# Kernel tuning notes

Measured on AMD Instinct MI355X. Metric: run time of the kernel, lower is better.

## Reference

```python
import jax, jax.numpy as jnp
import numpy as np

D_MODEL = 1024
N_HEADS = 16
D_K = D_MODEL // N_HEADS


def setup_inputs() -> dict:
    key = jax.random.key(0)
    ks = jax.random.split(key, 5)
    B, T = 4, 2048
    scale = 1.0 / np.sqrt(D_MODEL)
    return {
        "x": jax.random.normal(ks[0], (B, T, D_MODEL), dtype=jnp.float32),
        "W_q": jax.random.normal(ks[1], (D_MODEL, D_MODEL), dtype=jnp.float32) * scale,
        "W_k": jax.random.normal(ks[2], (D_MODEL, D_MODEL), dtype=jnp.float32) * scale,
        "W_v": jax.random.normal(ks[3], (D_MODEL, D_MODEL), dtype=jnp.float32) * scale,
        "W_o": jax.random.normal(ks[4], (D_MODEL, D_MODEL), dtype=jnp.float32) * scale,
    }


def reference(x, W_q, W_k, W_v, W_o):
    B, T, C = x.shape
    # torch nn.Linear(bias=False): y = x @ W.T
    def proj(W):
        y = jnp.einsum('btc,dc->btd', x, W)
        # (B, T, H, Dk) -> (B, H, T, Dk)
        return y.reshape(B, T, N_HEADS, D_K).transpose(0, 2, 1, 3)

    Q, K, V = proj(W_q), proj(W_k), proj(W_v)
    scores = jnp.einsum('bhqd,bhkd->bhqk', Q, K) / jnp.sqrt(jnp.float32(D_K))
    # causal mask: disallow k > q
    causal = jnp.triu(jnp.ones((T, T), dtype=bool), k=1)
    scores = jnp.where(causal, -jnp.inf, scores)
    attn = jax.nn.softmax(scores, axis=-1)
    out = jnp.einsum('bhqk,bhkd->bhqd', attn, V)  # (B, H, T, Dk)
    out = out.transpose(0, 2, 1, 3).reshape(B, T, C)
    return jnp.einsum('btc,dc->btd', out, W_o)
```

## Files before the change

kernel.cpp:

```cpp
#include <hip/hip_runtime.h>

typedef unsigned short u16;
typedef __attribute__((ext_vector_type(8))) short short8;
typedef __attribute__((ext_vector_type(4))) float f32x4;
typedef __attribute__((ext_vector_type(16))) float f32x16;

__device__ __forceinline__ u16 f2bf(float f) {
    union { float f; unsigned u; } v; v.f = f;
    unsigned r = v.u + 0x7fff + ((v.u >> 16) & 1);
    return (u16)(r >> 16);
}

__device__ __forceinline__ unsigned cvtpk(float lo, float hi) {
    unsigned r;
    asm("v_cvt_pk_bf16_f32 %0, %1, %2" : "=v"(r) : "v"(lo), "v"(hi));
    return r;
}

__device__ __forceinline__ void plswap(unsigned& a, unsigned& b) {
    auto r = __builtin_amdgcn_permlane32_swap((int)a, (int)b, false, false);
    a = (unsigned)r[0]; b = (unsigned)r[1];
}

__device__ __forceinline__ void gload_lds16(const void* g, void* l) {
    __builtin_amdgcn_global_load_lds(
        (const __attribute__((address_space(1))) void*)g,
        (__attribute__((address_space(3))) void*)l, 16, 0, 0);
}

__global__ __launch_bounds__(256) void cvt_all(
    const float* __restrict__ x, const float* __restrict__ wq, const float* __restrict__ wk,
    const float* __restrict__ wv, const float* __restrict__ wo,
    u16* __restrict__ xb, u16* __restrict__ wqb, u16* __restrict__ wkb,
    u16* __restrict__ wvb, u16* __restrict__ wob)
{
    const int b = blockIdx.x;
    const float* src; u16* dst; int base;
    if (b < 8192)       { src = x;  dst = xb;  base = b; }
    else if (b < 9216)  { src = wq; dst = wqb; base = b - 8192; }
    else if (b < 10240) { src = wk; dst = wkb; base = b - 9216; }
    else if (b < 11264) { src = wv; dst = wvb; base = b - 10240; }
    else                { src = wo; dst = wob; base = b - 11264; }
    const int i = base * 256 + threadIdx.x;
    float4 v = ((const float4*)src)[i];
    ushort4 o;
    o.x = f2bf(v.x); o.y = f2bf(v.y); o.z = f2bf(v.z); o.w = f2bf(v.w);
    ((ushort4*)dst)[i] = o;
}

__global__ __launch_bounds__(256, 2) void gemm_qkv(
    const u16* __restrict__ Agl, const u16* __restrict__ Wq, const u16* __restrict__ Wk,
    const u16* __restrict__ Wv, u16* __restrict__ Qo, u16* __restrict__ Ko, u16* __restrict__ Vo)
{
    __shared__ alignas(16) u16 As[2][128 * 64];
    __shared__ alignas(16) u16 Bs[2][128 * 64];
    const int tid = threadIdx.x;
    const int lane = tid & 63;
    const int w = tid >> 6;
    const int wr = w >> 1, wc = w & 1;
    const int bid = blockIdx.x;
    const int xcd = bid & 7;
    const int j   = bid >> 3;
    const int nb  = j & 7;
    const int rem = j >> 3;
    const int z   = rem >> 3;
    const int yb  = (xcd << 3) | (rem & 7);
    const int m0 = yb * 128;
    const int n0 = nb * 128;
    const u16* Bgl = (z == 0) ? Wq : (z == 1) ? Wk : Wv;

    f32x4 acc[4][4] = {};

    auto stage = [&](int buf, int kb) {
#pragma unroll
        for (int p = 0; p < 4; ++p) {
            const int row = p * 32 + (tid >> 3);
            const int ke = kb + (((tid & 7) * 8) ^ ((row & 7) * 8));
            gload_lds16(Agl + (size_t)(m0 + row) * 1024 + ke, (char*)As[buf] + p * 4096 + w * 1024);
            gload_lds16(Bgl + (size_t)(n0 + row) * 1024 + ke, (char*)Bs[buf] + p * 4096 + w * 1024);
        }
    };

    stage(0, 0);
    for (int kt = 0; kt < 16; ++kt) {
        const int cur = kt & 1;
        if (kt < 15) {
            stage(cur ^ 1, (kt + 1) * 64);
            asm volatile("s_waitcnt vmcnt(8)" ::: "memory");
        } else {
            asm volatile("s_waitcnt vmcnt(0)" ::: "memory");
        }
        __builtin_amdgcn_s_barrier();
        asm volatile("" ::: "memory");
#pragma unroll
        for (int ks = 0; ks < 2; ++ks) {
            short8 a[4], b[4];
#pragma unroll
            for (int m = 0; m < 4; ++m) {
                const int row = wr * 64 + m * 16 + (lane & 15);
                const int ke = (ks * 32 + (lane >> 4) * 8) ^ ((row & 7) * 8);
                a[m] = *(const short8*)(&As[cur][row * 64 + ke]);
            }
#pragma unroll
            for (int n = 0; n < 4; ++n) {
                const int row = wc * 64 + n * 16 + (lane & 15);
                const int ke = (ks * 32 + (lane >> 4) * 8) ^ ((row & 7) * 8);
                b[n] = *(const short8*)(&Bs[cur][row * 64 + ke]);
            }
#pragma unroll
            for (int m = 0; m < 4; ++m)
#pragma unroll
                for (int n = 0; n < 4; ++n)
                    acc[m][n] = __builtin_amdgcn_mfma_f32_16x16x32_bf16(a[m], b[n], acc[m][n], 0, 0, 0);
        }
        asm volatile("" ::: "memory");
        __builtin_amdgcn_s_barrier();
        asm volatile("" ::: "memory");
    }
    const float qs = (z == 0) ? 0.18033688011112043f : 1.0f;
#pragma unroll
    for (int m = 0; m < 4; ++m)
#pragma unroll
        for (int n = 0; n < 4; ++n)
#pragma unroll
            for (int r = 0; r < 4; ++r) {
                const int row = m0 + wr * 64 + m * 16 + ((lane >> 4) << 2) + r;
                const int col = n0 + wc * 64 + n * 16 + (lane & 15);
                const u16 bv = f2bf(acc[m][n][r] * qs);
                const int bb = row >> 11, t = row & 2047, h = col >> 6, dk = col & 63;
                if (z == 2) {
                    Vo[((size_t)(bb * 16 + h) * 64 + dk) * 2048 + t] = bv;
                } else {
                    u16* dst = (z == 0) ? Qo : Ko;
                    dst[(((size_t)(bb * 16 + h) * 2048 + t) << 6) + dk] = bv;
                }
            }
}

__global__ __launch_bounds__(256, 2) void gemm_out(
    const u16* __restrict__ Agl, const u16* __restrict__ Bgl, float* __restrict__ Co)
{
    __shared__ alignas(16) u16 As[2][128 * 64];
    __shared__ alignas(16) u16 Bs[2][128 * 64];
    const int tid = threadIdx.x;
    const int lane = tid & 63;
    const int w = tid >> 6;
    const int wr = w >> 1, wc = w & 1;
    const int bid = blockIdx.x;
    const int xcd = bid & 7;
    const int j   = bid >> 3;
    const int nb  = j & 7;
    const int yb  = (xcd << 3) | (j >> 3);
    const int m0 = yb * 128;
    const int n0 = nb * 128;

    f32x4 acc[4][4] = {};

    auto stage = [&](int buf, int kb) {
#pragma unroll
        for (int p = 0; p < 4; ++p) {
            const int row = p * 32 + (tid >> 3);
            const int ke = kb + (((tid & 7) * 8) ^ ((row & 7) * 8));
            gload_lds16(Agl + (size_t)(m0 + row) * 1024 + ke, (char*)As[buf] + p * 4096 + w * 1024);
            gload_lds16(Bgl + (size_t)(n0 + row) * 1024 + ke, (char*)Bs[buf] + p * 4096 + w * 1024);
        }
    };

    stage(0, 0);
    for (int kt = 0; kt < 16; ++kt) {
        const int cur = kt & 1;
        if (kt < 15) {
            stage(cur ^ 1, (kt + 1) * 64);
            asm volatile("s_waitcnt vmcnt(8)" ::: "memory");
        } else {
            asm volatile("s_waitcnt vmcnt(0)" ::: "memory");
        }
        __builtin_amdgcn_s_barrier();
        asm volatile("" ::: "memory");
#pragma unroll
        for (int ks = 0; ks < 2; ++ks) {
            short8 a[4], b[4];
#pragma unroll
            for (int m = 0; m < 4; ++m) {
                const int row = wr * 64 + m * 16 + (lane & 15);
                const int ke = (ks * 32 + (lane >> 4) * 8) ^ ((row & 7) * 8);
                a[m] = *(const short8*)(&As[cur][row * 64 + ke]);
            }
#pragma unroll
            for (int n = 0; n < 4; ++n) {
                const int row = wc * 64 + n * 16 + (lane & 15);
                const int ke = (ks * 32 + (lane >> 4) * 8) ^ ((row & 7) * 8);
                b[n] = *(const short8*)(&Bs[cur][row * 64 + ke]);
            }
#pragma unroll
            for (int m = 0; m < 4; ++m)
#pragma unroll
                for (int n = 0; n < 4; ++n)
                    acc[m][n] = __builtin_amdgcn_mfma_f32_16x16x32_bf16(a[m], b[n], acc[m][n], 0, 0, 0);
        }
        asm volatile("" ::: "memory");
        __builtin_amdgcn_s_barrier();
        asm volatile("" ::: "memory");
    }
#pragma unroll
    for (int m = 0; m < 4; ++m)
#pragma unroll
        for (int n = 0; n < 4; ++n)
#pragma unroll
            for (int r = 0; r < 4; ++r) {
                const int row = m0 + wr * 64 + m * 16 + ((lane >> 4) << 2) + r;
                const int col = n0 + wc * 64 + n * 16 + (lane & 15);
                Co[(size_t)row * 1024 + col] = acc[m][n][r];
            }
}

__global__ __launch_bounds__(256, 4) void attn_fwd2(
    const u16* __restrict__ Q, const u16* __restrict__ Kg,
    const u16* __restrict__ Vt, u16* __restrict__ O)
{
    __shared__ alignas(16) u16 Ks[2][64 * 64];
    __shared__ alignas(16) u16 Vs[2][64 * 64];
    __shared__ alignas(16) float abuf[4][32];

    const int tid = threadIdx.x;
    const int lane = tid & 63;
    const int w = tid >> 6;
    const int l31 = lane & 31;
    const int hi = lane >> 5;
    const int bid = blockIdx.x;
    const int s  = bid >> 8;
    const int g  = bid & 255;
    const int u  = g >> 3;
    const int bh = ((u & 7) << 3) | (g & 7);
    const int jj = u >> 3;
    const int p  = ((s >> 1) << 2) | jj;
    const int qc = (s & 1) ? p : (15 - p);
    const size_t hb = (size_t)bh << 17;
    const int bb = bh >> 4, h = bh & 15;

    const int q0 = qc * 128;
    const int wq0 = q0 + w * 32;
    const int ntiles = qc * 2 + 2;
    const int qrow = wq0 + l31;

    short8 qf[4];
#pragma unroll
    for (int ks = 0; ks < 4; ++ks)
        qf[ks] = *(const short8*)(&Q[hb + ((size_t)qrow << 6) + ks * 16 + hi * 8]);

    f32x16 o0 = {}, o1 = {};
    float lsum = 0.f;

#pragma unroll
    for (int pp = 0; pp < 2; ++pp) {
        const int c = pp * 256 + tid;
        const int row = c >> 3;
        const int ke = ((c & 7) * 8) ^ ((row & 7) * 8);
        gload_lds16(&Kg[hb + ((size_t)row << 6) + ke], (char*)Ks[0] + pp * 4096 + w * 1024);
        gload_lds16(&Vt[hb + ((size_t)row << 11) + ke], (char*)Vs[0] + pp * 4096 + w * 1024);
    }
    __syncthreads();

    for (int t = 0; t < ntiles; ++t) {
        const int cur = t & 1;
        if (t + 1 < ntiles) {
            const int t0n = (t + 1) * 64;
#pragma unroll
            for (int pp = 0; pp < 2; ++pp) {
                const int c = pp * 256 + tid;
                const int row = c >> 3;
                const int ke = ((c & 7) * 8) ^ ((row & 7) * 8);
                gload_lds16(&Kg[hb + ((size_t)(t0n + row) << 6) + ke], (char*)Ks[cur ^ 1] + pp * 4096 + w * 1024);
                gload_lds16(&Vt[hb + ((size_t)row << 11) + t0n + ke], (char*)Vs[cur ^ 1] + pp * 4096 + w * 1024);
            }
        }
        const int t0 = t * 64;
        if (t0 <= wq0 + 31) {
            const u16* ks_ = Ks[cur];
            const u16* vs_ = Vs[cur];
            const bool full1 = (t0 + 32 <= wq0 + 31);
            f32x16 s0 = {}, s1 = {};
            __builtin_amdgcn_s_setprio(1);
#pragma unroll
            for (int ks = 0; ks < 4; ++ks) {
                const int d0 = ks * 16 + hi * 8;
                const int r0 = l31;
                short8 kf0 = *(const short8*)(&ks_[r0 * 64 + (d0 ^ ((r0 & 7) * 8))]);
                s0 = __builtin_amdgcn_mfma_f32_32x32x16_bf16(kf0, qf[ks], s0, 0, 0, 0);
            }
            if (full1) {
#pragma unroll
                for (int ks = 0; ks < 4; ++ks) {
                    const int d0 = ks * 16 + hi * 8;
                    const int r1 = 32 + l31;
                    short8 kf1 = *(const short8*)(&ks_[r1 * 64 + (d0 ^ ((r1 & 7) * 8))]);
                    s1 = __builtin_amdgcn_mfma_f32_32x32x16_bf16(kf1, qf[ks], s1, 0, 0, 0);
                }
            }
            __builtin_amdgcn_s_setprio(0);
            if (t0 + 63 > wq0) {
#pragma unroll
                for (int r = 0; r < 16; ++r) {
                    const int kva = t0 + (r & 3) + 8 * (r >> 2) + 4 * hi;
                    if (kva > qrow)                s0[r] = -1e30f;
                    if (full1 && kva + 32 > qrow)  s1[r] = -1e30f;
                }
            }
            float rs = 0.f;
            unsigned pwv[16];
            const int nsl = full1 ? 4 : 2;
#pragma unroll
            for (int sl = 0; sl < 4; ++sl) {
                if (sl >= nsl) break;
                float pv[8];
#pragma unroll
                for (int i = 0; i < 8; ++i) {
                    const float sv = (sl < 2) ? s0[(sl & 1) * 8 + i] : s1[(sl & 1) * 8 + i];
                    pv[i] = exp2f(sv);
                    rs += pv[i];
                }
                unsigned w01 = cvtpk(pv[0], pv[1]);
                unsigned w23 = cvtpk(pv[2], pv[3]);
                unsigned w45 = cvtpk(pv[4], pv[5]);
                unsigned w67 = cvtpk(pv[6], pv[7]);
                plswap(w01, w45);
                plswap(w23, w67);
                pwv[sl * 4 + 0] = w01; pwv[sl * 4 + 1] = w23;
                pwv[sl * 4 + 2] = w45; pwv[sl * 4 + 3] = w67;
            }
            rs += __shfl_xor(rs, 32);
            lsum += rs;
            __builtin_amdgcn_s_setprio(1);
#pragma unroll
            for (int sl = 0; sl < 4; ++sl) {
                if (sl >= nsl) break;
                union { unsigned uu4[4]; short8 s8; } uu;
                uu.uu4[0] = pwv[sl * 4 + 0]; uu.uu4[1] = pwv[sl * 4 + 1];
                uu.uu4[2] = pwv[sl * 4 + 2]; uu.uu4[3] = pwv[sl * 4 + 3];
                const int tc = sl * 16 + hi * 8;
                const int r0 = l31, r1 = 32 + l31;
                short8 vf0 = *(const short8*)(&vs_[r0 * 64 + (tc ^ ((r0 & 7) * 8))]);
                short8 vf1 = *(const short8*)(&vs_[r1 * 64 + (tc ^ ((r1 & 7) * 8))]);
                o0 = __builtin_amdgcn_mfma_f32_32x32x16_bf16(uu.s8, vf0, o0, 0, 0, 0);
                o1 = __builtin_amdgcn_mfma_f32_32x32x16_bf16(uu.s8, vf1, o1, 0, 0, 0);
            }
            __builtin_amdgcn_s_setprio(0);
        }
        __syncthreads();
    }
    if (hi == 0) abuf[w][l31] = __builtin_amdgcn_rcpf(lsum);
#pragma unroll
    for (int c = 0; c < 4; ++c) {
        const f32x4 a4 = *(const f32x4*)(&abuf[w][c * 8 + hi * 4]);
#pragma unroll
        for (int e = 0; e < 4; ++e) {
            const int r = c * 4 + e;
            const int qr = wq0 + (r & 3) + 8 * (r >> 2) + 4 * hi;
            const size_t rb = ((size_t)(bb * 2048 + qr) << 10) + h * 64;
            O[rb + l31]      = f2bf(o0[r] * a4[e]);
            O[rb + 32 + l31] = f2bf(o1[r] * a4[e]);
        }
    }
}

extern "C" void kernel_launch(void* const* d_in, const int* in_sizes, int n_in,
                              void* d_out, int out_size, void* d_ws, size_t ws_size,
                              hipStream_t stream) {
    const float* x  = (const float*)d_in[0];
    const float* Wq = (const float*)d_in[1];
    const float* Wk = (const float*)d_in[2];
    const float* Wv = (const float*)d_in[3];
    const float* Wo = (const float*)d_in[4];
    char* ws = (char*)d_ws;
    const size_t MB = 1u << 20;
    u16* xb   = (u16*)(ws);
    u16* Ob   = (u16*)(ws);
    u16* wqb  = (u16*)(ws + 16 * MB);
    u16* wkb  = (u16*)(ws + 18 * MB);
    u16* wvb  = (u16*)(ws + 20 * MB);
    u16* wob  = (u16*)(ws + 22 * MB);
    u16* Qws  = (u16*)(ws + 24 * MB);
    u16* Kws  = (u16*)(ws + 40 * MB);
    u16* Vtws = (u16*)(ws + 56 * MB);

    cvt_all<<<12288, 256, 0, stream>>>(x, Wq, Wk, Wv, Wo, xb, wqb, wkb, wvb, wob);
    gemm_qkv<<<1536, 256, 0, stream>>>(xb, wqb, wkb, wvb, Qws, Kws, Vtws);
    attn_fwd2<<<1024, 256, 0, stream>>>(Qws, Kws, Vtws, Ob);
    gemm_out<<<512, 256, 0, stream>>>(Ob, wob, (float*)d_out);
}
```

Before: 240.3 us.

## Retile QKV GEMM to 256x256 blocks with 512 threads and deeper prefetch

Replaces the 128x128-tile QKV projection kernel with a 256x256-tile version that uses 8 waves per block and 128KB of dynamic LDS. This raises operand reuse per LDS load, cutting global and LDS traffic per FLOP. Global-to-LDS staging now runs two K-steps ahead instead of one, with the refill issued after the post-compute barrier. MFMA bursts are wrapped in s_setprio. The grid shrinks from 1536 to 384 blocks, which risks wave-quantization imbalance across CUs and lowers occupancy, since only one such block fits per CU.

```diff
diff --git a/kernel.cpp b/kernel.cpp
--- a/kernel.cpp
+++ b/kernel.cpp
@@ -48,85 +48,112 @@
     ((ushort4*)dst)[i] = o;
 }
 
-__global__ __launch_bounds__(256, 2) void gemm_qkv(
+__global__ __launch_bounds__(512, 2) void gemm_qkv256(
     const u16* __restrict__ Agl, const u16* __restrict__ Wq, const u16* __restrict__ Wk,
     const u16* __restrict__ Wv, u16* __restrict__ Qo, u16* __restrict__ Ko, u16* __restrict__ Vo)
 {
-    __shared__ alignas(16) u16 As[2][128 * 64];
-    __shared__ alignas(16) u16 Bs[2][128 * 64];
+    extern __shared__ char smem[];
+    char* AsB = smem;
+    char* BsB = smem + 65536;
+
     const int tid = threadIdx.x;
     const int lane = tid & 63;
     const int w = tid >> 6;
-    const int wr = w >> 1, wc = w & 1;
+    const int wr = w >> 2;
+    const int wc = w & 3;
     const int bid = blockIdx.x;
     const int xcd = bid & 7;
     const int j   = bid >> 3;
-    const int nb  = j & 7;
-    const int rem = j >> 3;
-    const int z   = rem >> 3;
-    const int yb  = (xcd << 3) | (rem & 7);
-    const int m0 = yb * 128;
-    const int n0 = nb * 128;
+    const int nb  = j & 3;
+    const int my  = (j >> 2) & 3;
+    const int z   = j >> 4;
+    const int yb  = (xcd << 2) | my;
+    const int m0 = yb * 256;
+    const int n0 = nb * 256;
     const u16* Bgl = (z == 0) ? Wq : (z == 1) ? Wk : Wv;
 
-    f32x4 acc[4][4] = {};
+    f32x4 acc[8][4] = {};
 
     auto stage = [&](int buf, int kb) {
 #pragma unroll
-        for (int p = 0; p < 4; ++p) {
-            const int row = p * 32 + (tid >> 3);
-            const int ke = kb + (((tid & 7) * 8) ^ ((row & 7) * 8));
-            gload_lds16(Agl + (size_t)(m0 + row) * 1024 + ke, (char*)As[buf] + p * 4096 + w * 1024);
-            gload_lds16(Bgl + (size_t)(n0 + row) * 1024 + ke, (char*)Bs[buf] + p * 4096 + w * 1024);
+        for (int g = 0; g < 4; ++g) {
+            const int p = g * 8192 + tid * 16;
+            const int row = p >> 7;
+            const int sg = ((p & 127) >> 4) ^ (row & 7);
+            gload_lds16(Agl + (size_t)(m0 + row) * 1024 + kb + sg * 8, AsB + buf * 32768 + p);
+        }
+#pragma unroll
+        for (int g = 0; g < 4; ++g) {
+            const int p = g * 8192 + tid * 16;
+            const int row = p >> 7;
+            const int sg = ((p & 127) >> 4) ^ (row & 7);
+            gload_lds16(Bgl + (size_t)(n0 + row) * 1024 + kb + sg * 8, BsB + buf * 32768 + p);
         }
     };
 
     stage(0, 0);
+    stage(1, 64);
     for (int kt = 0; kt < 16; ++kt) {
         const int cur = kt & 1;
         if (kt < 15) {
-            stage(cur ^ 1, (kt + 1) * 64);
             asm volatile("s_waitcnt vmcnt(8)" ::: "memory");
         } else {
             asm volatile("s_waitcnt vmcnt(0)" ::: "memory");
         }
         __builtin_amdgcn_s_barrier();
         asm volatile("" ::: "memory");
-#pragma unroll
-        for (int ks = 0; ks < 2; ++ks) {
-            short8 a[4], b[4];
-#pragma unroll
-            for (int m = 0; m < 4; ++m) {
-                const int row = wr * 64 + m * 16 + (lane & 15);
+
+        const u16* Ab = (const u16*)(AsB + cur * 32768);
+        const u16* Bb = (const u16*)(BsB + cur * 32768);
+
+        short8 bfr[4][2];
+#pragma unroll
+        for (int ni = 0; ni < 4; ++ni)
+#pragma unroll
+            for (int ks = 0; ks < 2; ++ks) {
+                const int row = wc * 64 + ni * 16 + (lane & 15);
                 const int ke = (ks * 32 + (lane >> 4) * 8) ^ ((row & 7) * 8);
-                a[m] = *(const short8*)(&As[cur][row * 64 + ke]);
-            }
-#pragma unroll
-            for (int n = 0; n < 4; ++n) {
-                const int row = wc * 64 + n * 16 + (lane & 15);
-                const int ke = (ks * 32 + (lane >> 4) * 8) ^ ((row & 7) * 8);
-                b[n] = *(const short8*)(&Bs[cur][row * 64 + ke]);
-            }
-#pragma unroll
-            for (int m = 0; m < 4; ++m)
-#pragma unroll
-                for (int n = 0; n < 4; ++n)
-                    acc[m][n] = __builtin_amdgcn_mfma_f32_16x16x32_bf16(a[m], b[n], acc[m][n], 0, 0, 0);
-        }
+                bfr[ni][ks] = *(const short8*)(&Bb[row * 64 + ke]);
+            }
+#pragma unroll
+        for (int p = 0; p < 4; ++p) {
+            short8 afr[2][2];
+#pragma unroll
+            for (int mm = 0; mm < 2; ++mm)
+#pragma unroll
+                for (int ks = 0; ks < 2; ++ks) {
+                    const int row = wr * 128 + (p * 2 + mm) * 16 + (lane & 15);
+                    const int ke = (ks * 32 + (lane >> 4) * 8) ^ ((row & 7) * 8);
+                    afr[mm][ks] = *(const short8*)(&Ab[row * 64 + ke]);
+                }
+            __builtin_amdgcn_s_setprio(1);
+#pragma unroll
+            for (int mm = 0; mm < 2; ++mm)
+#pragma unroll
+                for (int ni = 0; ni < 4; ++ni)
+#pragma unroll
+                    for (int ks = 0; ks < 2; ++ks)
+                        acc[p * 2 + mm][ni] = __builtin_amdgcn_mfma_f32_16x16x32_bf16(
+                            afr[mm][ks], bfr[ni][ks], acc[p * 2 + mm][ni], 0, 0, 0);
+            __builtin_amdgcn_s_setprio(0);
+        }
+
         asm volatile("" ::: "memory");
         __builtin_amdgcn_s_barrier();
         asm volatile("" ::: "memory");
+        if (kt + 2 < 16) stage(cur, (kt + 2) * 64);
     }
+
     const float qs = (z == 0) ? 0.18033688011112043f : 1.0f;
 #pragma unroll
-    for (int m = 0; m < 4; ++m)
-#pragma unroll
-        for (int n = 0; n < 4; ++n)
+    for (int mi = 0; mi < 8; ++mi)
+#pragma unroll
+        for (int ni = 0; ni < 4; ++ni)
 #pragma unroll
             for (int r = 0; r < 4; ++r) {
-                const int row = m0 + wr * 64 + m * 16 + ((lane >> 4) << 2) + r;
-                const int col = n0 + wc * 64 + n * 16 + (lane & 15);
-                const u16 bv = f2bf(acc[m][n][r] * qs);
+                const int row = m0 + wr * 128 + mi * 16 + ((lane >> 4) << 2) + r;
+                const int col = n0 + wc * 64 + ni * 16 + (lane & 15);
+                const u16 bv = f2bf(acc[mi][ni][r] * qs);
                 const int bb = row >> 11, t = row & 2047, h = col >> 6, dk = col & 63;
                 if (z == 2) {
                     Vo[((size_t)(bb * 16 + h) * 64 + dk) * 2048 + t] = bv;
@@ -383,8 +410,11 @@
     u16* Kws  = (u16*)(ws + 40 * MB);
     u16* Vtws = (u16*)(ws + 56 * MB);
 
+    hipFuncSetAttribute((const void*)gemm_qkv256,
+                        hipFuncAttributeMaxDynamicSharedMemorySize, 131072);
+
     cvt_all<<<12288, 256, 0, stream>>>(x, Wq, Wk, Wv, Wo, xb, wqb, wkb, wvb, wob);
-    gemm_qkv<<<1536, 256, 0, stream>>>(xb, wqb, wkb, wvb, Qws, Kws, Vtws);
+    gemm_qkv256<<<384, 512, 131072, stream>>>(xb, wqb, wkb, wvb, Qws, Kws, Vtws);
     attn_fwd2<<<1024, 256, 0, stream>>>(Qws, Kws, Vtws, Ob);
     gemm_out<<<512, 256, 0, stream>>>(Ob, wob, (float*)d_out);
 }
```

New measurement: 261.2 us. 1.09x slower.

## Rewrite QKV GEMM with 256x256 tiles, 8 waves and 4-stage LDS pipeline

Applied to the files above, without the earlier changes.

Replaces the 128x128 double-buffered QKV projection GEMM with a 256x256-tile kernel using 512 threads (8 waves), a K-step of 32 and a 4-slot ring buffer in 128KB of dynamic LDS. Global loads for step kt+3 are interleaved between the two MFMA halves of each step, and s_setprio raises priority during MFMA bursts. The aim is more data reuse per tile and better overlap of memory traffic with compute. In exchange it uses large LDS per block with fewer blocks (384), which limits occupancy and may leave CUs underused.

```diff
diff --git a/kernel.cpp b/kernel.cpp
--- a/kernel.cpp
+++ b/kernel.cpp
@@ -48,85 +48,126 @@
     ((ushort4*)dst)[i] = o;
 }
 
-__global__ __launch_bounds__(256, 2) void gemm_qkv(
+__global__ __launch_bounds__(512, 2) void gemm_qkv8p(
     const u16* __restrict__ Agl, const u16* __restrict__ Wq, const u16* __restrict__ Wk,
     const u16* __restrict__ Wv, u16* __restrict__ Qo, u16* __restrict__ Ko, u16* __restrict__ Vo)
 {
-    __shared__ alignas(16) u16 As[2][128 * 64];
-    __shared__ alignas(16) u16 Bs[2][128 * 64];
+    extern __shared__ char smem[];
     const int tid = threadIdx.x;
     const int lane = tid & 63;
     const int w = tid >> 6;
-    const int wr = w >> 1, wc = w & 1;
+    const int wr = w >> 2;
+    const int wc = w & 3;
     const int bid = blockIdx.x;
     const int xcd = bid & 7;
     const int j   = bid >> 3;
-    const int nb  = j & 7;
-    const int rem = j >> 3;
-    const int z   = rem >> 3;
-    const int yb  = (xcd << 3) | (rem & 7);
-    const int m0 = yb * 128;
-    const int n0 = nb * 128;
+    const int my  = j & 3;
+    const int nb  = j >> 2;
+    const int m0  = ((xcd << 2) | my) * 256;
+    const int z   = nb >> 2;
+    const int n0  = (nb & 3) * 256;
     const u16* Bgl = (z == 0) ? Wq : (z == 1) ? Wk : Wv;
 
-    f32x4 acc[4][4] = {};
-
-    auto stage = [&](int buf, int kb) {
-#pragma unroll
-        for (int p = 0; p < 4; ++p) {
-            const int row = p * 32 + (tid >> 3);
-            const int ke = kb + (((tid & 7) * 8) ^ ((row & 7) * 8));
-            gload_lds16(Agl + (size_t)(m0 + row) * 1024 + ke, (char*)As[buf] + p * 4096 + w * 1024);
-            gload_lds16(Bgl + (size_t)(n0 + row) * 1024 + ke, (char*)Bs[buf] + p * 4096 + w * 1024);
+    f32x4 acc[8][4] = {};
+
+    auto stage_kt = [&](int kt, int tensor) {
+        const u16* src = tensor ? Bgl : Agl;
+        const int t0 = tensor ? n0 : m0;
+        char* base = smem + tensor * 65536 + (kt & 3) * 16384;
+#pragma unroll
+        for (int g2 = 0; g2 < 2; ++g2) {
+            const int p = g2 * 8192 + tid * 16;
+            const int rp = p >> 7;
+            const int qs = (p & 127) >> 4;
+            const int lr = qs ^ (rp & 7);
+            const int row = rp * 2 + (lr >> 2);
+            const int ge = (lr & 3) * 8;
+            gload_lds16(src + (size_t)(t0 + row) * 1024 + kt * 32 + ge, base + p);
         }
     };
 
-    stage(0, 0);
-    for (int kt = 0; kt < 16; ++kt) {
-        const int cur = kt & 1;
-        if (kt < 15) {
-            stage(cur ^ 1, (kt + 1) * 64);
-            asm volatile("s_waitcnt vmcnt(8)" ::: "memory");
-        } else {
-            asm volatile("s_waitcnt vmcnt(0)" ::: "memory");
-        }
-        __builtin_amdgcn_s_barrier();
-        asm volatile("" ::: "memory");
-#pragma unroll
-        for (int ks = 0; ks < 2; ++ks) {
-            short8 a[4], b[4];
-#pragma unroll
-            for (int m = 0; m < 4; ++m) {
-                const int row = wr * 64 + m * 16 + (lane & 15);
-                const int ke = (ks * 32 + (lane >> 4) * 8) ^ ((row & 7) * 8);
-                a[m] = *(const short8*)(&As[cur][row * 64 + ke]);
-            }
-#pragma unroll
-            for (int n = 0; n < 4; ++n) {
-                const int row = wc * 64 + n * 16 + (lane & 15);
-                const int ke = (ks * 32 + (lane >> 4) * 8) ^ ((row & 7) * 8);
-                b[n] = *(const short8*)(&Bs[cur][row * 64 + ke]);
-            }
-#pragma unroll
-            for (int m = 0; m < 4; ++m)
-#pragma unroll
-                for (int n = 0; n < 4; ++n)
-                    acc[m][n] = __builtin_amdgcn_mfma_f32_16x16x32_bf16(a[m], b[n], acc[m][n], 0, 0, 0);
-        }
-        asm volatile("" ::: "memory");
-        __builtin_amdgcn_s_barrier();
-        asm volatile("" ::: "memory");
+#define KSTEP(KT, DOSTAGE, VMS)                                                  \
+    {                                                                            \
+        const int slot_ = (KT) & 3;                                              \
+        const u16* Asl = (const u16*)(smem + slot_ * 16384);                     \
+        const u16* Bsl = (const u16*)(smem + 65536 + slot_ * 16384);             \
+        short8 bf_[4], af_[4];                                                   \
+        _Pragma("unroll")                                                        \
+        for (int ni = 0; ni < 4; ++ni) {                                         \
+            const int r = wc * 64 + ni * 16 + (lane & 15);                       \
+            const int rp = r >> 1;                                               \
+            const int q = (((r & 1) << 2) | (lane >> 4)) ^ (rp & 7);             \
+            bf_[ni] = *(const short8*)(Bsl + rp * 64 + q * 8);                   \
+        }                                                                        \
+        _Pragma("unroll")                                                        \
+        for (int mi = 0; mi < 4; ++mi) {                                         \
+            const int r = wr * 128 + mi * 16 + (lane & 15);                      \
+            const int rp = r >> 1;                                               \
+            const int q = (((r & 1) << 2) | (lane >> 4)) ^ (rp & 7);             \
+            af_[mi] = *(const short8*)(Asl + rp * 64 + q * 8);                   \
+        }                                                                        \
+        if (DOSTAGE) stage_kt((KT) + 3, 0);                                      \
+        __builtin_amdgcn_s_barrier();                                            \
+        asm volatile("" ::: "memory");                                           \
+        __builtin_amdgcn_s_setprio(1);                                           \
+        _Pragma("unroll")                                                        \
+        for (int mi = 0; mi < 4; ++mi)                                           \
+            _Pragma("unroll")                                                    \
+            for (int ni = 0; ni < 4; ++ni)                                       \
+                acc[mi][ni] = __builtin_amdgcn_mfma_f32_16x16x32_bf16(           \
+                    af_[mi], bf_[ni], acc[mi][ni], 0, 0, 0);                     \
+        __builtin_amdgcn_s_setprio(0);                                           \
+        asm volatile("" ::: "memory");                                           \
+        __builtin_amdgcn_s_barrier();                                            \
+        asm volatile("" ::: "memory");                                           \
+        _Pragma("unroll")                                                        \
+        for (int mi = 0; mi < 4; ++mi) {                                         \
+            const int r = wr * 128 + (mi + 4) * 16 + (lane & 15);                \
+            const int rp = r >> 1;                                               \
+            const int q = (((r & 1) << 2) | (lane >> 4)) ^ (rp & 7);             \
+            af_[mi] = *(const short8*)(Asl + rp * 64 + q * 8);                   \
+        }                                                                        \
+        if (DOSTAGE) stage_kt((KT) + 3, 1);                                      \
+        __builtin_amdgcn_s_barrier();                                            \
+        asm volatile("" ::: "memory");                                           \
+        __builtin_amdgcn_s_setprio(1);                                           \
+        _Pragma("unroll")                                                        \
+        for (int mi = 0; mi < 4; ++mi)                                           \
+            _Pragma("unroll")                                                    \
+            for (int ni = 0; ni < 4; ++ni)                                       \
+                acc[mi + 4][ni] = __builtin_amdgcn_mfma_f32_16x16x32_bf16(       \
+                    af_[mi], bf_[ni], acc[mi + 4][ni], 0, 0, 0);                 \
+        __builtin_amdgcn_s_setprio(0);                                           \
+        VMS;                                                                     \
+        asm volatile("" ::: "memory");                                           \
+        __builtin_amdgcn_s_barrier();                                            \
+        asm volatile("" ::: "memory");                                           \
     }
+
+    stage_kt(0, 0); stage_kt(0, 1);
+    stage_kt(1, 0); stage_kt(1, 1);
+    stage_kt(2, 0); stage_kt(2, 1);
+    asm volatile("s_waitcnt vmcnt(8)" ::: "memory");
+    __builtin_amdgcn_s_barrier();
+    asm volatile("" ::: "memory");
+
+    for (int kt = 0; kt < 29; ++kt)
+        KSTEP(kt, true, asm volatile("s_waitcnt vmcnt(8)" ::: "memory"))
+    KSTEP(29, false, asm volatile("s_waitcnt vmcnt(4)" ::: "memory"))
+    KSTEP(30, false, asm volatile("s_waitcnt vmcnt(0)" ::: "memory"))
+    KSTEP(31, false, (void)0)
+#undef KSTEP
+
     const float qs = (z == 0) ? 0.18033688011112043f : 1.0f;
 #pragma unroll
-    for (int m = 0; m < 4; ++m)
-#pragma unroll
-        for (int n = 0; n < 4; ++n)
+    for (int mi = 0; mi < 8; ++mi)
+#pragma unroll
+        for (int ni = 0; ni < 4; ++ni)
 #pragma unroll
             for (int r = 0; r < 4; ++r) {
-                const int row = m0 + wr * 64 + m * 16 + ((lane >> 4) << 2) + r;
-                const int col = n0 + wc * 64 + n * 16 + (lane & 15);
-                const u16 bv = f2bf(acc[m][n][r] * qs);
+                const int row = m0 + wr * 128 + mi * 16 + ((lane >> 4) << 2) + r;
+                const int col = n0 + wc * 64 + ni * 16 + (lane & 15);
+                const u16 bv = f2bf(acc[mi][ni][r] * qs);
                 const int bb = row >> 11, t = row & 2047, h = col >> 6, dk = col & 63;
                 if (z == 2) {
                     Vo[((size_t)(bb * 16 + h) * 64 + dk) * 2048 + t] = bv;
@@ -383,8 +424,11 @@
     u16* Kws  = (u16*)(ws + 40 * MB);
     u16* Vtws = (u16*)(ws + 56 * MB);
 
+    hipFuncSetAttribute((const void*)gemm_qkv8p,
+                        hipFuncAttributeMaxDynamicSharedMemorySize, 131072);
+
     cvt_all<<<12288, 256, 0, stream>>>(x, Wq, Wk, Wv, Wo, xb, wqb, wkb, wvb, wob);
-    gemm_qkv<<<1536, 256, 0, stream>>>(xb, wqb, wkb, wvb, Qws, Kws, Vtws);
+    gemm_qkv8p<<<384, 512, 131072, stream>>>(xb, wqb, wkb, wvb, Qws, Kws, Vtws);
     attn_fwd2<<<1024, 256, 0, stream>>>(Qws, Kws, Vtws, Ob);
     gemm_out<<<512, 256, 0, stream>>>(Ob, wob, (float*)d_out);
 }
```

After: 261.8 us. 1.09x slower.
